# Kernel tuning notes

Hardware: AMD Instinct MI355X
Metric: run time of the kernel (lower is better)

Reference implementation:

```python
import jax, jax.numpy as jnp
import numpy as np

GAMMA = 0.9865
B, S, D = 8, 2048, 128


def setup_inputs() -> dict:
    key = jax.random.key(0)
    kq, kk, kv, kw = jax.random.split(key, 4)
    xq = jax.random.normal(kq, (B, S, D), dtype=jnp.float32)
    xk = jax.random.normal(kk, (B, S, D), dtype=jnp.float32)
    xv = jax.random.normal(kv, (B, S, D), dtype=jnp.float32)
    # NOTE: the original builds three Dense layers by repeating the SAME object,
    # so Q/K/V share a single no-bias weight matrix W.
    W = jax.random.normal(kw, (D, D), dtype=jnp.float32) * (1.0 / np.sqrt(D))
    return {"xq": xq, "xk": xk, "xv": xv, "W": W}


def _decay_matrix(seq_len, gamma):
    # Original: factors[i,j] = gamma^(i-j); keep upper triangle (j>=i); transpose.
    # Result: Dm[n,m] = gamma^(m-n) for n >= m, else 0 (lower triangular).
    n = jnp.arange(seq_len, dtype=jnp.float32)
    expo = n[None, :] - n[:, None]            # [S,S], entry (n,m) = m - n
    Dm = jnp.tril(jnp.float32(gamma) ** expo)  # zero out m > n before they'd matter
    return Dm


def reference(xq, xk, xv, W):
    Q = xq @ W
    K = xk @ W
    V = xv @ W
    d = Q.shape[-1]
    scores = jnp.einsum('bnd,bmd->bnm', Q, K) / jnp.sqrt(jnp.float32(d))
    Dm = _decay_matrix(Q.shape[1], GAMMA)
    # D /= reduce_sum(D, axis=1) ** 0.5  -> row-sums broadcast over LAST axis,
    # i.e. column m of D is divided by sqrt(rowsum[m]). Faithful to tf broadcasting.
    Dm = Dm / jnp.sqrt(jnp.sum(Dm, axis=1))
    scores = scores * Dm
    # per-batch norm: xs[n,m] / max(|sum_k xs[m,k]|, 1)  (tf broadcasting over last axis)
    s = jnp.sum(scores, axis=2)                       # [B,S]
    scores = scores / jnp.maximum(jnp.abs(s), 1.0)[:, None, :]
    return scores @ V
```

## Files before the change

kernel.cpp:

```cpp
#include <hip/hip_runtime.h>
#include <math.h>


constexpr int B = 8, S = 2048, D = 128;
constexpr int C = 64, NC = S / C;
constexpr int BS = B * S;
constexpr int NCH = B * NC;
#define GAMMA_F 0.9865f

typedef __attribute__((ext_vector_type(8))) short short8;
typedef __attribute__((ext_vector_type(8))) unsigned short ushort8;
typedef __attribute__((ext_vector_type(4))) float f32x4;

__device__ inline unsigned short f2bf(float f) {
  unsigned u = __builtin_bit_cast(unsigned, f);
  return (unsigned short)((u + 0x7FFF + ((u >> 16) & 1)) >> 16);
}
__device__ inline float bf2f(unsigned short h) {
  return __builtin_bit_cast(float, (unsigned)h << 16);
}

__global__ void k_init(const float* __restrict__ W, unsigned short* __restrict__ wt,
                       float* __restrict__ qs, float* __restrict__ ks) {
  int bid = blockIdx.x, tid = threadIdx.x;
  if (bid < 64) {
    int idx = bid * 256 + tid;
    int k = idx & 127, c = idx >> 7;
    wt[c * 128 + k] = f2bf(W[k * 128 + c]);
  } else {
    int n = (bid - 64) * 256 + tid;
    if (n < S) {
      double g = (double)GAMMA_F;
      double lg = log(g);
      double gmn = exp(-lg * (double)n);
      double gn  = exp(lg * (double)n);
      double ginv = 1.0 / g;
      double rs = (exp(log(ginv) * (double)(n + 1)) - 1.0) / (ginv - 1.0);
      qs[n] = (float)(gmn / sqrt(128.0));
      ks[n] = (float)(gn / sqrt(rs));
    }
  }
}

__global__ __launch_bounds__(256) void k_proj(
    const float* __restrict__ xq, const float* __restrict__ xk,
    const float* __restrict__ xv, const unsigned short* __restrict__ wt,
    const float* __restrict__ qs, const float* __restrict__ ks,
    unsigned short* __restrict__ qb, unsigned short* __restrict__ kb,
    unsigned short* __restrict__ vb, float* __restrict__ cs) {
  __shared__ float css[4][128];
  int mat = blockIdx.y;
  const float* X = (mat == 0) ? xq : ((mat == 1) ? xk : xv);
  unsigned short* Ob = (mat == 0) ? qb : ((mat == 1) ? kb : vb);

  int tid = threadIdx.x, w = tid >> 6, lane = tid & 63;
  int bc = blockIdx.x;
  int r0 = bc * 64 + w * 16;
  int arow = r0 + (lane & 15);
  int kg = (lane >> 4) * 8;

  f32x4 acc[8];
#pragma unroll
  for (int j = 0; j < 8; j++) acc[j] = (f32x4){0.f, 0.f, 0.f, 0.f};

#pragma unroll
  for (int t = 0; t < 4; t++) {
    int k0 = t * 32 + kg;
    const float* ap = X + (size_t)arow * 128 + k0;
    float a8[8];
    *(f32x4*)(a8) = *(const f32x4*)ap;
    *(f32x4*)(a8 + 4) = *(const f32x4*)(ap + 4);
    short8 af;
#pragma unroll
    for (int i = 0; i < 8; i++) af[i] = (short)f2bf(a8[i]);
#pragma unroll
    for (int j = 0; j < 8; j++) {
      short8 bf = *(const short8*)(wt + (size_t)(j * 16 + (lane & 15)) * 128 + k0);
      acc[j] = __builtin_amdgcn_mfma_f32_16x16x32_bf16(af, bf, acc[j], 0, 0, 0);
    }
  }
  int crow = r0 + (lane >> 4) * 4;
  float csp[8];
#pragma unroll
  for (int j = 0; j < 8; j++) csp[j] = 0.f;
#pragma unroll
  for (int rr = 0; rr < 4; rr++) {
    int row = crow + rr;
    int n = row & (S - 1);
    float sc = (mat == 0) ? qs[n] : ((mat == 1) ? ks[n] : 1.0f);
#pragma unroll
    for (int j = 0; j < 8; j++) {
      float v = acc[j][rr] * sc;
      Ob[(size_t)row * 128 + j * 16 + (lane & 15)] = f2bf(v);
      csp[j] += v;
    }
  }
  if (mat == 1) {
#pragma unroll
    for (int j = 0; j < 8; j++) {
      csp[j] += __shfl_xor(csp[j], 16);
      csp[j] += __shfl_xor(csp[j], 32);
    }
    if ((lane >> 4) == 0)
#pragma unroll
      for (int j = 0; j < 8; j++) css[w][j * 16 + lane] = csp[j];
  }
  __syncthreads();
  if (mat == 1 && tid < 128)
    cs[bc * 128 + tid] = css[0][tid] + css[1][tid] + css[2][tid] + css[3][tid];
}

__global__ __launch_bounds__(256) void k_mid(
    const unsigned short* __restrict__ qb, const unsigned short* __restrict__ kb,
    const unsigned short* __restrict__ vb, const float* __restrict__ cs,
    unsigned short* __restrict__ al, unsigned short* __restrict__ vbT,
    unsigned short* __restrict__ Hc) {
  __shared__ unsigned short kraw[64][136];
  __shared__ unsigned short kT[128][72];
  __shared__ unsigned short vT[128][72];
  __shared__ float csp[128];
  __shared__ float invl[64];
  int bc = blockIdx.x, b = bc >> 5, c = bc & 31;
  int tid = threadIdx.x, w = tid >> 6, lane = tid & 63;
  size_t base = (size_t)bc * C * D;
  int kg = (lane >> 4) * 8;
  int arow = w * 16 + (lane & 15);
  int crow = w * 16 + (lane >> 4) * 4;

  if (tid < 128) {
    float a = 0.f;
    for (int cc = 0; cc < c; cc++) a += cs[(size_t)(b * NC + cc) * D + tid];
    csp[tid] = a;
  }

  f32x4 a1[4];
#pragma unroll
  for (int m = 0; m < 4; m++) a1[m] = (f32x4){0.f, 0.f, 0.f, 0.f};
#pragma unroll
  for (int t = 0; t < 4; t++) {
    int k0 = t * 32 + kg;
    short8 af = *(const short8*)(qb + base + (size_t)arow * D + k0);
#pragma unroll
    for (int mt = 0; mt < 4; mt++) {
      short8 bf = *(const short8*)(kb + base + (size_t)(mt * 16 + (lane & 15)) * D + k0);
      a1[mt] = __builtin_amdgcn_mfma_f32_16x16x32_bf16(af, bf, a1[mt], 0, 0, 0);
    }
  }
  unsigned short* alg = al + (size_t)bc * 64 * 64;
  float rsum[4] = {0.f, 0.f, 0.f, 0.f};
#pragma unroll
  for (int mt = 0; mt < 4; mt++)
#pragma unroll
    for (int rr = 0; rr < 4; rr++) {
      int n_l = crow + rr, m_l = mt * 16 + (lane & 15);
      float mv = (n_l >= m_l) ? a1[mt][rr] : 0.f;
      alg[n_l * 64 + m_l] = f2bf(mv);
      rsum[rr] += mv;
    }
#pragma unroll
  for (int rr = 0; rr < 4; rr++) {
    float r = rsum[rr];
    r += __shfl_xor(r, 1); r += __shfl_xor(r, 2);
    r += __shfl_xor(r, 4); r += __shfl_xor(r, 8);
    rsum[rr] = r;
  }
  __syncthreads();
#pragma unroll
  for (int rr = 0; rr < 4; rr++) {
    int row = crow + rr;
    ushort8 q8 = *(const ushort8*)(qb + base + (size_t)row * D + (lane & 15) * 8);
    float dt = 0.f;
#pragma unroll
    for (int ii = 0; ii < 8; ii++) dt += bf2f(q8[ii]) * csp[(lane & 15) * 8 + ii];
    dt += __shfl_xor(dt, 1); dt += __shfl_xor(dt, 2);
    dt += __shfl_xor(dt, 4); dt += __shfl_xor(dt, 8);
    if ((lane & 15) == 0) invl[row] = 1.f / fmaxf(fabsf(rsum[rr] + dt), 1.f);
  }
#pragma unroll
  for (int i = 0; i < 4; i++) {
    int e = (i * 256 + tid) * 8;
    *(ushort8*)&kraw[e >> 7][e & 127] = *(const ushort8*)(kb + base + e);
  }
  __syncthreads();
  {
    int d = tid & 127, mh = tid >> 7;
#pragma unroll
    for (int mg = 0; mg < 4; mg++) {
      ushort8 pk;
#pragma unroll
      for (int i = 0; i < 8; i++) pk[i] = kraw[mh * 32 + mg * 8 + i][d];
      *(ushort8*)&kT[d][mh * 32 + mg * 8] = pk;
    }
  }
  __syncthreads();
#pragma unroll
  for (int i = 0; i < 4; i++) {
    int e = (i * 256 + tid) * 8;
    int row = e >> 7, col = e & 127;
    ushort8 v8 = *(const ushort8*)(vb + base + e);
    float inv = invl[row];
    ushort8 o;
#pragma unroll
    for (int ii = 0; ii < 8; ii++) o[ii] = f2bf(bf2f(v8[ii]) * inv);
    *(ushort8*)&kraw[row][col] = o;
  }
  __syncthreads();
  {
    int d = tid & 127, mh = tid >> 7;
#pragma unroll
    for (int mg = 0; mg < 4; mg++) {
      ushort8 pk;
#pragma unroll
      for (int i = 0; i < 8; i++) pk[i] = kraw[mh * 32 + mg * 8 + i][d];
      *(ushort8*)&vT[d][mh * 32 + mg * 8] = pk;
    }
  }
  __syncthreads();
  f32x4 acc[2][8];
#pragma unroll
  for (int i = 0; i < 2; i++)
#pragma unroll
    for (int j = 0; j < 8; j++) acc[i][j] = (f32x4){0.f, 0.f, 0.f, 0.f};
#pragma unroll
  for (int t = 0; t < 2; t++) {
    int k0 = t * 32 + kg;
    short8 a2[2];
#pragma unroll
    for (int i = 0; i < 2; i++)
      a2[i] = *(const short8*)&vT[w * 32 + i * 16 + (lane & 15)][k0];
#pragma unroll
    for (int j = 0; j < 8; j++) {
      short8 bf = *(const short8*)&kT[j * 16 + (lane & 15)][k0];
#pragma unroll
      for (int i = 0; i < 2; i++)
        acc[i][j] = __builtin_amdgcn_mfma_f32_16x16x32_bf16(a2[i], bf, acc[i][j], 0, 0, 0);
    }
  }
  unsigned short* g = Hc + (size_t)bc * D * D;
#pragma unroll
  for (int i = 0; i < 2; i++)
#pragma unroll
    for (int j = 0; j < 8; j++)
#pragma unroll
      for (int rr = 0; rr < 4; rr++)
        g[(size_t)(w * 32 + i * 16 + (lane >> 4) * 4 + rr) * D + j * 16 + (lane & 15)] =
            f2bf(acc[i][j][rr]);
  {
    int d = tid >> 1, pp = (tid & 1) * 32;
    unsigned short* dst = vbT + (size_t)bc * D * C + (size_t)d * C + pp;
#pragma unroll
    for (int q8i = 0; q8i < 4; q8i++)
      *(ushort8*)(dst + q8i * 8) = *(ushort8*)&vT[d][pp + q8i * 8];
  }
}

__global__ __launch_bounds__(64) void k_gscan(const unsigned short* __restrict__ Hc,
                                              unsigned short* __restrict__ HS) {
  int b = blockIdx.x, gy = blockIdx.y, t = threadIdx.x;
  int d2 = gy * 4 + (t >> 4), d1 = (t & 15) * 8;
  size_t off = ((size_t)(b * NC) * D + d2) * D + d1;
  ushort8 v[NC];
#pragma unroll
  for (int c = 0; c < NC; c++)
    v[c] = *(const ushort8*)(Hc + off + (size_t)c * D * D);
  float run[8];
#pragma unroll
  for (int j = 0; j < 8; j++) run[j] = 0.f;
#pragma unroll
  for (int c = 0; c < NC; c++) {
    ushort8 o;
#pragma unroll
    for (int j = 0; j < 8; j++) {
      o[j] = f2bf(run[j]);
      run[j] += bf2f(v[c][j]);
    }
    *(ushort8*)(HS + off + (size_t)c * D * D) = o;
  }
}

__global__ __launch_bounds__(256) void k_out(
    const unsigned short* __restrict__ qb, const unsigned short* __restrict__ al,
    const unsigned short* __restrict__ vbT, const unsigned short* __restrict__ HS,
    float* __restrict__ out) {
  int bc = blockIdx.x, tid = threadIdx.x, w = tid >> 6, lane = tid & 63;
  size_t base = (size_t)bc * C * D;
  int kg = (lane >> 4) * 8;
  int arow = w * 16 + (lane & 15);
  int crow = w * 16 + (lane >> 4) * 4;

  f32x4 acc[8];
#pragma unroll
  for (int j = 0; j < 8; j++) acc[j] = (f32x4){0.f, 0.f, 0.f, 0.f};
  const unsigned short* hrow = HS + (size_t)bc * D * D;
#pragma unroll
  for (int t = 0; t < 4; t++) {
    int k0 = t * 32 + kg;
    short8 af = *(const short8*)(qb + base + (size_t)arow * D + k0);
#pragma unroll
    for (int j = 0; j < 8; j++) {
      short8 bf = *(const short8*)(hrow + (size_t)(j * 16 + (lane & 15)) * D + k0);
      acc[j] = __builtin_amdgcn_mfma_f32_16x16x32_bf16(af, bf, acc[j], 0, 0, 0);
    }
  }
  const unsigned short* alg = al + (size_t)bc * 64 * 64;
  const unsigned short* vt = vbT + (size_t)bc * D * C;
#pragma unroll
  for (int t = 0; t < 2; t++) {
    int k0 = t * 32 + kg;
    short8 af = *(const short8*)(alg + (size_t)arow * 64 + k0);
#pragma unroll
    for (int j = 0; j < 8; j++) {
      short8 bf = *(const short8*)(vt + (size_t)(j * 16 + (lane & 15)) * C + k0);
      acc[j] = __builtin_amdgcn_mfma_f32_16x16x32_bf16(af, bf, acc[j], 0, 0, 0);
    }
  }
#pragma unroll
  for (int j = 0; j < 8; j++)
#pragma unroll
    for (int rr = 0; rr < 4; rr++)
      out[base + (size_t)(crow + rr) * D + j * 16 + (lane & 15)] = acc[j][rr];
}

extern "C" void kernel_launch(void* const* d_in, const int* in_sizes, int n_in,
                              void* d_out, int out_size, void* d_ws, size_t ws_size,
                              hipStream_t stream) {
  const float* xq = (const float*)d_in[0];
  const float* xk = (const float*)d_in[1];
  const float* xv = (const float*)d_in[2];
  const float* W  = (const float*)d_in[3];
  float* out = (float*)d_out;

  char* p = (char*)d_ws;
  unsigned short* qb  = (unsigned short*)p;  p += (size_t)BS * D * 2;
  unsigned short* kb  = (unsigned short*)p;  p += (size_t)BS * D * 2;
  unsigned short* vb  = (unsigned short*)p;  p += (size_t)BS * D * 2;
  unsigned short* vbT = (unsigned short*)p;  p += (size_t)NCH * D * C * 2;
  unsigned short* al  = (unsigned short*)p;  p += (size_t)NCH * C * C * 2;
  unsigned short* Hc  = (unsigned short*)p;  p += (size_t)NCH * D * D * 2;
  unsigned short* HS  = (unsigned short*)p;  p += (size_t)NCH * D * D * 2;
  unsigned short* wt  = (unsigned short*)p;  p += (size_t)D * D * 2;
  float* cs = (float*)p;                     p += (size_t)NCH * D * 4;
  float* qs = (float*)p;                     p += (size_t)S * 4;
  float* ks = (float*)p;                     p += (size_t)S * 4;

  hipLaunchKernelGGL(k_init, dim3(72), dim3(256), 0, stream, W, wt, qs, ks);
  hipLaunchKernelGGL(k_proj, dim3(NCH, 3), dim3(256), 0, stream,
                     xq, xk, xv, wt, qs, ks, qb, kb, vb, cs);
  hipLaunchKernelGGL(k_mid, dim3(NCH), dim3(256), 0, stream, qb, kb, vb, cs, al, vbT, Hc);
  hipLaunchKernelGGL(k_gscan, dim3(B, 32), dim3(64), 0, stream, Hc, HS);
  hipLaunchKernelGGL(k_out, dim3(NCH), dim3(256), 0, stream, qb, al, vbT, HS, out);
}
```

Measured before the change: 59.71 us.

## Fuse all stages into one cooperative persistent kernel with grid syncs

Replaces the five-launch pipeline (init, projection, mid, scan, output) with a single cooperative kernel of 256 blocks. Each block keeps its chunk's Q/K/V, the transposed W, the intra-chunk attention tile and the transposed V in LDS, and uses grid.sync between phases. This removes launch overhead and the global round-trips of the q/k/v/al/vT intermediates. In exchange it adds three grid-wide barriers, recomputes the W transpose in every block, and computes the decay scales in float instead of double. The old multi-kernel path is kept as a fallback if the cooperative launch fails.

```diff
diff --git a/kernel.cpp b/kernel.cpp
--- a/kernel.cpp
+++ b/kernel.cpp
@@ -1,5 +1,8 @@
 #include <hip/hip_runtime.h>
+#include <hip/hip_cooperative_groups.h>
 #include <math.h>
+
+namespace cg = cooperative_groups;
 
 
 constexpr int B = 8, S = 2048, D = 128;
@@ -20,8 +23,273 @@
   return __builtin_bit_cast(float, (unsigned)h << 16);
 }
 
-__global__ void k_init(const float* __restrict__ W, unsigned short* __restrict__ wt,
-                       float* __restrict__ qs, float* __restrict__ ks) {
+__global__ __launch_bounds__(256, 1) void k_fused(
+    const float* __restrict__ xq, const float* __restrict__ xk,
+    const float* __restrict__ xv, const float* __restrict__ W,
+    float* __restrict__ cs, unsigned short* __restrict__ Hc,
+    unsigned short* __restrict__ HS, float* __restrict__ out) {
+  __shared__ unsigned short qkv[3][64][136];
+  __shared__ alignas(16) char ovl[34816];
+  __shared__ unsigned short vT[128][72];
+  __shared__ float csp[128];
+  __shared__ float invl[64];
+  __shared__ float css[4][128];
+  auto wt = (unsigned short(*)[136])ovl;
+  auto kT = (unsigned short(*)[72])ovl;
+  auto al = (unsigned short(*)[72])(ovl + 18432);
+
+  cg::grid_group grid = cg::this_grid();
+  int bc = blockIdx.x, b = bc >> 5, c = bc & 31;
+  int tid = threadIdx.x, w = tid >> 6, lane = tid & 63;
+  int l15 = lane & 15;
+  int kg = (lane >> 4) * 8;
+  int arow = w * 16 + l15;
+  int crow = w * 16 + (lane >> 4) * 4;
+
+  for (int idx = tid; idx < 128 * 128; idx += 256) {
+    int cc = idx >> 7, k = idx & 127;
+    wt[cc][k] = f2bf(W[k * 128 + cc]);
+  }
+  float lgf = logf(GAMMA_F);
+  __syncthreads();
+
+  for (int mat = 0; mat < 3; mat++) {
+    const float* X = (mat == 0) ? xq : ((mat == 1) ? xk : xv);
+    f32x4 acc[8];
+#pragma unroll
+    for (int j = 0; j < 8; j++) acc[j] = (f32x4){0.f, 0.f, 0.f, 0.f};
+#pragma unroll
+    for (int t = 0; t < 4; t++) {
+      int k0 = t * 32 + kg;
+      const float* ap = X + (size_t)(bc * 64 + arow) * 128 + k0;
+      float a8[8];
+      *(f32x4*)(a8) = *(const f32x4*)ap;
+      *(f32x4*)(a8 + 4) = *(const f32x4*)(ap + 4);
+      short8 af;
+#pragma unroll
+      for (int i = 0; i < 8; i++) af[i] = (short)f2bf(a8[i]);
+#pragma unroll
+      for (int j = 0; j < 8; j++) {
+        short8 bf = *(const short8*)&wt[j * 16 + l15][k0];
+        acc[j] = __builtin_amdgcn_mfma_f32_16x16x32_bf16(af, bf, acc[j], 0, 0, 0);
+      }
+    }
+    float cacc[8];
+#pragma unroll
+    for (int j = 0; j < 8; j++) cacc[j] = 0.f;
+#pragma unroll
+    for (int rr = 0; rr < 4; rr++) {
+      int row = crow + rr;
+      int n = (bc * 64 + row) & (S - 1);
+      float sc;
+      if (mat == 0) {
+        sc = expf(-lgf * (float)n) * 0.088388347f;
+      } else if (mat == 1) {
+        float rs = (expf(-lgf * (float)(n + 1)) - 1.f) * (GAMMA_F / (1.f - GAMMA_F));
+        sc = expf(lgf * (float)n) / sqrtf(rs);
+      } else {
+        sc = 1.f;
+      }
+#pragma unroll
+      for (int j = 0; j < 8; j++) {
+        float v = acc[j][rr] * sc;
+        qkv[mat][row][j * 16 + l15] = f2bf(v);
+        if (mat == 1) cacc[j] += v;
+      }
+    }
+    if (mat == 1) {
+#pragma unroll
+      for (int j = 0; j < 8; j++) {
+        cacc[j] += __shfl_xor(cacc[j], 16);
+        cacc[j] += __shfl_xor(cacc[j], 32);
+      }
+      if ((lane >> 4) == 0)
+#pragma unroll
+        for (int j = 0; j < 8; j++) css[w][j * 16 + lane] = cacc[j];
+      __syncthreads();
+      if (tid < 128)
+        cs[(size_t)bc * 128 + tid] = css[0][tid] + css[1][tid] + css[2][tid] + css[3][tid];
+    }
+  }
+  grid.sync();
+
+  if (tid < 128) {
+    float a = 0.f;
+    for (int cc = 0; cc < c; cc++) a += cs[(size_t)(b * NC + cc) * 128 + tid];
+    csp[tid] = a;
+  }
+  f32x4 a1[4];
+#pragma unroll
+  for (int m = 0; m < 4; m++) a1[m] = (f32x4){0.f, 0.f, 0.f, 0.f};
+#pragma unroll
+  for (int t = 0; t < 4; t++) {
+    int k0 = t * 32 + kg;
+    short8 af = *(const short8*)&qkv[0][arow][k0];
+#pragma unroll
+    for (int mt = 0; mt < 4; mt++) {
+      short8 bf = *(const short8*)&qkv[1][mt * 16 + l15][k0];
+      a1[mt] = __builtin_amdgcn_mfma_f32_16x16x32_bf16(af, bf, a1[mt], 0, 0, 0);
+    }
+  }
+  float rsum[4] = {0.f, 0.f, 0.f, 0.f};
+#pragma unroll
+  for (int mt = 0; mt < 4; mt++)
+#pragma unroll
+    for (int rr = 0; rr < 4; rr++) {
+      int n_l = crow + rr, m_l = mt * 16 + l15;
+      float mv = (n_l >= m_l) ? a1[mt][rr] : 0.f;
+      al[n_l][m_l] = f2bf(mv);
+      rsum[rr] += mv;
+    }
+#pragma unroll
+  for (int rr = 0; rr < 4; rr++) {
+    float r = rsum[rr];
+    r += __shfl_xor(r, 1); r += __shfl_xor(r, 2);
+    r += __shfl_xor(r, 4); r += __shfl_xor(r, 8);
+    rsum[rr] = r;
+  }
+  __syncthreads();
+#pragma unroll
+  for (int rr = 0; rr < 4; rr++) {
+    int row = crow + rr;
+    ushort8 q8 = *(const ushort8*)&qkv[0][row][l15 * 8];
+    float dt = 0.f;
+#pragma unroll
+    for (int ii = 0; ii < 8; ii++) dt += bf2f(q8[ii]) * csp[l15 * 8 + ii];
+    dt += __shfl_xor(dt, 1); dt += __shfl_xor(dt, 2);
+    dt += __shfl_xor(dt, 4); dt += __shfl_xor(dt, 8);
+    if (l15 == 0) invl[row] = 1.f / fmaxf(fabsf(rsum[rr] + dt), 1.f);
+  }
+  {
+    int d = tid & 127, mh = tid >> 7;
+#pragma unroll
+    for (int mg = 0; mg < 4; mg++) {
+      ushort8 pk;
+#pragma unroll
+      for (int i = 0; i < 8; i++) pk[i] = qkv[1][mh * 32 + mg * 8 + i][d];
+      *(ushort8*)&kT[d][mh * 32 + mg * 8] = pk;
+    }
+  }
+  __syncthreads();
+#pragma unroll
+  for (int i = 0; i < 4; i++) {
+    int e = (i * 256 + tid) * 8;
+    int row = e >> 7, col = e & 127;
+    ushort8 v8 = *(const ushort8*)&qkv[2][row][col];
+    float inv = invl[row];
+    ushort8 o;
+#pragma unroll
+    for (int ii = 0; ii < 8; ii++) o[ii] = f2bf(bf2f(v8[ii]) * inv);
+    *(ushort8*)&qkv[2][row][col] = o;
+  }
+  __syncthreads();
+  {
+    int d = tid & 127, mh = tid >> 7;
+#pragma unroll
+    for (int mg = 0; mg < 4; mg++) {
+      ushort8 pk;
+#pragma unroll
+      for (int i = 0; i < 8; i++) pk[i] = qkv[2][mh * 32 + mg * 8 + i][d];
+      *(ushort8*)&vT[d][mh * 32 + mg * 8] = pk;
+    }
+  }
+  __syncthreads();
+  {
+    f32x4 hacc[2][8];
+#pragma unroll
+    for (int i = 0; i < 2; i++)
+#pragma unroll
+      for (int j = 0; j < 8; j++) hacc[i][j] = (f32x4){0.f, 0.f, 0.f, 0.f};
+#pragma unroll
+    for (int t = 0; t < 2; t++) {
+      int k0 = t * 32 + kg;
+      short8 a2[2];
+#pragma unroll
+      for (int i = 0; i < 2; i++)
+        a2[i] = *(const short8*)&vT[w * 32 + i * 16 + l15][k0];
+#pragma unroll
+      for (int j = 0; j < 8; j++) {
+        short8 bf = *(const short8*)&kT[j * 16 + l15][k0];
+#pragma unroll
+        for (int i = 0; i < 2; i++)
+          hacc[i][j] = __builtin_amdgcn_mfma_f32_16x16x32_bf16(a2[i], bf, hacc[i][j], 0, 0, 0);
+      }
+    }
+    unsigned short* g = Hc + (size_t)bc * D * D;
+#pragma unroll
+    for (int i = 0; i < 2; i++)
+#pragma unroll
+      for (int j = 0; j < 8; j++)
+#pragma unroll
+        for (int rr = 0; rr < 4; rr++)
+          g[(size_t)(w * 32 + i * 16 + (lane >> 4) * 4 + rr) * D + j * 16 + l15] =
+              f2bf(hacc[i][j][rr]);
+  }
+  grid.sync();
+
+  {
+    int d2 = c * 4 + (tid >> 6);
+    int s16 = tid & 63;
+    if (s16 < 16) {
+      int d1 = s16 * 8;
+      size_t off = ((size_t)(b * NC) * D + d2) * D + d1;
+      ushort8 v[NC];
+#pragma unroll
+      for (int c2 = 0; c2 < NC; c2++)
+        v[c2] = *(const ushort8*)(Hc + off + (size_t)c2 * D * D);
+      float run[8];
+#pragma unroll
+      for (int j = 0; j < 8; j++) run[j] = 0.f;
+#pragma unroll
+      for (int c2 = 0; c2 < NC; c2++) {
+        ushort8 o;
+#pragma unroll
+        for (int j = 0; j < 8; j++) {
+          o[j] = f2bf(run[j]);
+          run[j] += bf2f(v[c2][j]);
+        }
+        *(ushort8*)(HS + off + (size_t)c2 * D * D) = o;
+      }
+    }
+  }
+  grid.sync();
+
+  {
+    f32x4 oacc[8];
+#pragma unroll
+    for (int j = 0; j < 8; j++) oacc[j] = (f32x4){0.f, 0.f, 0.f, 0.f};
+    const unsigned short* hrow = HS + (size_t)bc * D * D;
+#pragma unroll
+    for (int t = 0; t < 4; t++) {
+      int k0 = t * 32 + kg;
+      short8 af = *(const short8*)&qkv[0][arow][k0];
+#pragma unroll
+      for (int j = 0; j < 8; j++) {
+        short8 bf = *(const short8*)(hrow + (size_t)(j * 16 + l15) * D + k0);
+        oacc[j] = __builtin_amdgcn_mfma_f32_16x16x32_bf16(af, bf, oacc[j], 0, 0, 0);
+      }
+    }
+#pragma unroll
+    for (int t = 0; t < 2; t++) {
+      int k0 = t * 32 + kg;
+      short8 af = *(const short8*)&al[arow][k0];
+#pragma unroll
+      for (int j = 0; j < 8; j++) {
+        short8 bf = *(const short8*)&vT[j * 16 + l15][k0];
+        oacc[j] = __builtin_amdgcn_mfma_f32_16x16x32_bf16(af, bf, oacc[j], 0, 0, 0);
+      }
+    }
+    size_t base = (size_t)bc * C * D;
+#pragma unroll
+    for (int j = 0; j < 8; j++)
+#pragma unroll
+      for (int rr = 0; rr < 4; rr++)
+        out[base + (size_t)(crow + rr) * D + j * 16 + l15] = oacc[j][rr];
+  }
+}
+
+__global__ void fb_init(const float* __restrict__ W, unsigned short* __restrict__ wt,
+                        float* __restrict__ qs, float* __restrict__ ks) {
   int bid = blockIdx.x, tid = threadIdx.x;
   if (bid < 64) {
     int idx = bid * 256 + tid;
@@ -42,7 +310,7 @@
   }
 }
 
-__global__ __launch_bounds__(256) void k_proj(
+__global__ __launch_bounds__(256) void fb_proj(
     const float* __restrict__ xq, const float* __restrict__ xk,
     const float* __restrict__ xv, const unsigned short* __restrict__ wt,
     const float* __restrict__ qs, const float* __restrict__ ks,
@@ -62,7 +330,6 @@
   f32x4 acc[8];
 #pragma unroll
   for (int j = 0; j < 8; j++) acc[j] = (f32x4){0.f, 0.f, 0.f, 0.f};
-
 #pragma unroll
   for (int t = 0; t < 4; t++) {
     int k0 = t * 32 + kg;
@@ -110,7 +377,7 @@
     cs[bc * 128 + tid] = css[0][tid] + css[1][tid] + css[2][tid] + css[3][tid];
 }
 
-__global__ __launch_bounds__(256) void k_mid(
+__global__ __launch_bounds__(256) void fb_mid(
     const unsigned short* __restrict__ qb, const unsigned short* __restrict__ kb,
     const unsigned short* __restrict__ vb, const float* __restrict__ cs,
     unsigned short* __restrict__ al, unsigned short* __restrict__ vbT,
@@ -129,10 +396,9 @@
 
   if (tid < 128) {
     float a = 0.f;
-    for (int cc = 0; cc < c; cc++) a += cs[(size_t)(b * NC + cc) * D + tid];
+    for (int cc = 0; cc < c; cc++) a += cs[(size_t)(b * NC + cc) * 128 + tid];
     csp[tid] = a;
   }
-
   f32x4 a1[4];
 #pragma unroll
   for (int m = 0; m < 4; m++) a1[m] = (f32x4){0.f, 0.f, 0.f, 0.f};
@@ -254,8 +520,8 @@
   }
 }
 
-__global__ __launch_bounds__(64) void k_gscan(const unsigned short* __restrict__ Hc,
-                                              unsigned short* __restrict__ HS) {
+__global__ __launch_bounds__(64) void fb_gscan(const unsigned short* __restrict__ Hc,
+                                               unsigned short* __restrict__ HS) {
   int b = blockIdx.x, gy = blockIdx.y, t = threadIdx.x;
   int d2 = gy * 4 + (t >> 4), d1 = (t & 15) * 8;
   size_t off = ((size_t)(b * NC) * D + d2) * D + d1;
@@ -278,7 +544,7 @@
   }
 }
 
-__global__ __launch_bounds__(256) void k_out(
+__global__ __launch_bounds__(256) void fb_out(
     const unsigned short* __restrict__ qb, const unsigned short* __restrict__ al,
     const unsigned short* __restrict__ vbT, const unsigned short* __restrict__ HS,
     float* __restrict__ out) {
@@ -331,11 +597,14 @@
   float* out = (float*)d_out;
 
   char* p = (char*)d_ws;
+  float* cs_m = (float*)p;                   p += (size_t)NCH * D * 4;
+  unsigned short* Hc_m = (unsigned short*)p; p += (size_t)NCH * D * D * 2;
+  unsigned short* HS_m = (unsigned short*)p; p += (size_t)NCH * D * D * 2;
   unsigned short* qb  = (unsigned short*)p;  p += (size_t)BS * D * 2;
   unsigned short* kb  = (unsigned short*)p;  p += (size_t)BS * D * 2;
   unsigned short* vb  = (unsigned short*)p;  p += (size_t)BS * D * 2;
   unsigned short* vbT = (unsigned short*)p;  p += (size_t)NCH * D * C * 2;
-  unsigned short* al  = (unsigned short*)p;  p += (size_t)NCH * C * C * 2;
+  unsigned short* alg = (unsigned short*)p;  p += (size_t)NCH * C * C * 2;
   unsigned short* Hc  = (unsigned short*)p;  p += (size_t)NCH * D * D * 2;
   unsigned short* HS  = (unsigned short*)p;  p += (size_t)NCH * D * D * 2;
   unsigned short* wt  = (unsigned short*)p;  p += (size_t)D * D * 2;
@@ -343,10 +612,17 @@
   float* qs = (float*)p;                     p += (size_t)S * 4;
   float* ks = (float*)p;                     p += (size_t)S * 4;
 
-  hipLaunchKernelGGL(k_init, dim3(72), dim3(256), 0, stream, W, wt, qs, ks);
-  hipLaunchKernelGGL(k_proj, dim3(NCH, 3), dim3(256), 0, stream,
-                     xq, xk, xv, wt, qs, ks, qb, kb, vb, cs);
-  hipLaunchKernelGGL(k_mid, dim3(NCH), dim3(256), 0, stream, qb, kb, vb, cs, al, vbT, Hc);
-  hipLaunchKernelGGL(k_gscan, dim3(B, 32), dim3(64), 0, stream, Hc, HS);
-  hipLaunchKernelGGL(k_out, dim3(NCH), dim3(256), 0, stream, qb, al, vbT, HS, out);
-}
+  void* args[] = {(void*)&xq, (void*)&xk, (void*)&xv, (void*)&W,
+                  (void*)&cs_m, (void*)&Hc_m, (void*)&HS_m, (void*)&out};
+  hipError_t e = hipLaunchCooperativeKernel((const void*)k_fused, dim3(NCH),
+                                            dim3(256), args, 0, stream);
+  if (e != hipSuccess) {
+    hipLaunchKernelGGL(fb_init, dim3(72), dim3(256), 0, stream, W, wt, qs, ks);
+    hipLaunchKernelGGL(fb_proj, dim3(NCH, 3), dim3(256), 0, stream,
+                       xq, xk, xv, wt, qs, ks, qb, kb, vb, cs);
+    hipLaunchKernelGGL(fb_mid, dim3(NCH), dim3(256), 0, stream, qb, kb, vb, cs,
+                       alg, vbT, Hc);
+    hipLaunchKernelGGL(fb_gscan, dim3(B, 32), dim3(64), 0, stream, Hc, HS);
+    hipLaunchKernelGGL(fb_out, dim3(NCH), dim3(256), 0, stream, qb, alg, vbT, HS, out);
+  }
+}
```

Measured after the change: 141.3 us. 137% more time.

## Double threads per block in k_mid and k_out, splitting MFMA tiles across eight waves

Applied to the files above, without the earlier changes.

Raises k_mid and k_out from 256 to 512 threads per block. The score, Hc and output MFMA tiles are re-partitioned so each of the eight waves computes half as many tiles, and row sums are reduced through shared memory. The aim is more parallelism per block, since the grid has only 256 blocks on a device with many CUs, and shorter per-wave serial chains. The cost is extra shared-memory reduction and less operand reuse per wave.

```diff
diff --git a/kernel.cpp b/kernel.cpp
--- a/kernel.cpp
+++ b/kernel.cpp
@@ -62,7 +62,6 @@
   f32x4 acc[8];
 #pragma unroll
   for (int j = 0; j < 8; j++) acc[j] = (f32x4){0.f, 0.f, 0.f, 0.f};
-
 #pragma unroll
   for (int t = 0; t < 4; t++) {
     int k0 = t * 32 + kg;
@@ -110,7 +109,7 @@
     cs[bc * 128 + tid] = css[0][tid] + css[1][tid] + css[2][tid] + css[3][tid];
 }
 
-__global__ __launch_bounds__(256) void k_mid(
+__global__ __launch_bounds__(512) void k_mid(
     const unsigned short* __restrict__ qb, const unsigned short* __restrict__ kb,
     const unsigned short* __restrict__ vb, const float* __restrict__ cs,
     unsigned short* __restrict__ al, unsigned short* __restrict__ vbT,
@@ -120,82 +119,94 @@
   __shared__ unsigned short vT[128][72];
   __shared__ float csp[128];
   __shared__ float invl[64];
+  __shared__ float rsum_l[2][64];
   int bc = blockIdx.x, b = bc >> 5, c = bc & 31;
   int tid = threadIdx.x, w = tid >> 6, lane = tid & 63;
+  int l15 = lane & 15;
+  int kg = (lane >> 4) * 8;
   size_t base = (size_t)bc * C * D;
-  int kg = (lane >> 4) * 8;
-  int arow = w * 16 + (lane & 15);
-  int crow = w * 16 + (lane >> 4) * 4;
 
   if (tid < 128) {
     float a = 0.f;
-    for (int cc = 0; cc < c; cc++) a += cs[(size_t)(b * NC + cc) * D + tid];
+    for (int cc = 0; cc < c; cc++) a += cs[(size_t)(b * NC + cc) * 128 + tid];
     csp[tid] = a;
   }
 
-  f32x4 a1[4];
-#pragma unroll
-  for (int m = 0; m < 4; m++) a1[m] = (f32x4){0.f, 0.f, 0.f, 0.f};
-#pragma unroll
-  for (int t = 0; t < 4; t++) {
-    int k0 = t * 32 + kg;
-    short8 af = *(const short8*)(qb + base + (size_t)arow * D + k0);
-#pragma unroll
-    for (int mt = 0; mt < 4; mt++) {
-      short8 bf = *(const short8*)(kb + base + (size_t)(mt * 16 + (lane & 15)) * D + k0);
-      a1[mt] = __builtin_amdgcn_mfma_f32_16x16x32_bf16(af, bf, a1[mt], 0, 0, 0);
-    }
-  }
-  unsigned short* alg = al + (size_t)bc * 64 * 64;
-  float rsum[4] = {0.f, 0.f, 0.f, 0.f};
-#pragma unroll
-  for (int mt = 0; mt < 4; mt++)
+  {
+    int rt = w & 3, mh = w >> 2;
+    int arow = rt * 16 + l15;
+    int crow = rt * 16 + (lane >> 4) * 4;
+    f32x4 a1[2];
+#pragma unroll
+    for (int mi = 0; mi < 2; mi++) a1[mi] = (f32x4){0.f, 0.f, 0.f, 0.f};
+#pragma unroll
+    for (int t = 0; t < 4; t++) {
+      int k0 = t * 32 + kg;
+      short8 af = *(const short8*)(qb + base + (size_t)arow * D + k0);
+#pragma unroll
+      for (int mi = 0; mi < 2; mi++) {
+        int mt = mh * 2 + mi;
+        short8 bf = *(const short8*)(kb + base + (size_t)(mt * 16 + l15) * D + k0);
+        a1[mi] = __builtin_amdgcn_mfma_f32_16x16x32_bf16(af, bf, a1[mi], 0, 0, 0);
+      }
+    }
+    unsigned short* alg = al + (size_t)bc * 64 * 64;
+    float rsp[4] = {0.f, 0.f, 0.f, 0.f};
+#pragma unroll
+    for (int mi = 0; mi < 2; mi++)
+#pragma unroll
+      for (int rr = 0; rr < 4; rr++) {
+        int n_l = crow + rr, m_l = (mh * 2 + mi) * 16 + l15;
+        float mv = (n_l >= m_l) ? a1[mi][rr] : 0.f;
+        alg[n_l * 64 + m_l] = f2bf(mv);
+        rsp[rr] += mv;
+      }
 #pragma unroll
     for (int rr = 0; rr < 4; rr++) {
-      int n_l = crow + rr, m_l = mt * 16 + (lane & 15);
-      float mv = (n_l >= m_l) ? a1[mt][rr] : 0.f;
-      alg[n_l * 64 + m_l] = f2bf(mv);
-      rsum[rr] += mv;
-    }
-#pragma unroll
-  for (int rr = 0; rr < 4; rr++) {
-    float r = rsum[rr];
-    r += __shfl_xor(r, 1); r += __shfl_xor(r, 2);
-    r += __shfl_xor(r, 4); r += __shfl_xor(r, 8);
-    rsum[rr] = r;
-  }
-  __syncthreads();
-#pragma unroll
-  for (int rr = 0; rr < 4; rr++) {
-    int row = crow + rr;
-    ushort8 q8 = *(const ushort8*)(qb + base + (size_t)row * D + (lane & 15) * 8);
-    float dt = 0.f;
-#pragma unroll
-    for (int ii = 0; ii < 8; ii++) dt += bf2f(q8[ii]) * csp[(lane & 15) * 8 + ii];
-    dt += __shfl_xor(dt, 1); dt += __shfl_xor(dt, 2);
-    dt += __shfl_xor(dt, 4); dt += __shfl_xor(dt, 8);
-    if ((lane & 15) == 0) invl[row] = 1.f / fmaxf(fabsf(rsum[rr] + dt), 1.f);
-  }
-#pragma unroll
-  for (int i = 0; i < 4; i++) {
-    int e = (i * 256 + tid) * 8;
+      float r = rsp[rr];
+      r += __shfl_xor(r, 1); r += __shfl_xor(r, 2);
+      r += __shfl_xor(r, 4); r += __shfl_xor(r, 8);
+      if (l15 == 0) rsum_l[mh][crow + rr] = r;
+    }
+  }
+#pragma unroll
+  for (int i = 0; i < 2; i++) {
+    int e = (i * 512 + tid) * 8;
     *(ushort8*)&kraw[e >> 7][e & 127] = *(const ushort8*)(kb + base + e);
   }
   __syncthreads();
-  {
-    int d = tid & 127, mh = tid >> 7;
-#pragma unroll
-    for (int mg = 0; mg < 4; mg++) {
+
+  {
+    int row = tid >> 3, part = tid & 7;
+    const unsigned short* q = qb + base + (size_t)row * D + part * 16;
+    ushort8 q8a = *(const ushort8*)q;
+    ushort8 q8b = *(const ushort8*)(q + 8);
+    float dot = 0.f;
+#pragma unroll
+    for (int ii = 0; ii < 8; ii++) {
+      dot = fmaf(bf2f(q8a[ii]), csp[part * 16 + ii], dot);
+      dot = fmaf(bf2f(q8b[ii]), csp[part * 16 + 8 + ii], dot);
+    }
+    dot += __shfl_xor(dot, 1); dot += __shfl_xor(dot, 2); dot += __shfl_xor(dot, 4);
+    if (part == 0) {
+      float s = rsum_l[0][row] + rsum_l[1][row] + dot;
+      invl[row] = 1.f / fmaxf(fabsf(s), 1.f);
+    }
+  }
+  {
+    int d = tid & 127, mh2 = tid >> 7;
+#pragma unroll
+    for (int mg = 0; mg < 2; mg++) {
       ushort8 pk;
 #pragma unroll
-      for (int i = 0; i < 8; i++) pk[i] = kraw[mh * 32 + mg * 8 + i][d];
-      *(ushort8*)&kT[d][mh * 32 + mg * 8] = pk;
-    }
-  }
-  __syncthreads();
-#pragma unroll
-  for (int i = 0; i < 4; i++) {
-    int e = (i * 256 + tid) * 8;
+      for (int i = 0; i < 8; i++) pk[i] = kraw[mh2 * 16 + mg * 8 + i][d];
+      *(ushort8*)&kT[d][mh2 * 16 + mg * 8] = pk;
+    }
+  }
+  __syncthreads();
+#pragma unroll
+  for (int i = 0; i < 2; i++) {
+    int e = (i * 512 + tid) * 8;
     int row = e >> 7, col = e & 127;
     ushort8 v8 = *(const ushort8*)(vb + base + e);
     float inv = invl[row];
@@ -206,51 +217,43 @@
   }
   __syncthreads();
   {
-    int d = tid & 127, mh = tid >> 7;
-#pragma unroll
-    for (int mg = 0; mg < 4; mg++) {
+    int d = tid & 127, mh2 = tid >> 7;
+#pragma unroll
+    for (int mg = 0; mg < 2; mg++) {
       ushort8 pk;
 #pragma unroll
-      for (int i = 0; i < 8; i++) pk[i] = kraw[mh * 32 + mg * 8 + i][d];
-      *(ushort8*)&vT[d][mh * 32 + mg * 8] = pk;
-    }
-  }
-  __syncthreads();
-  f32x4 acc[2][8];
-#pragma unroll
-  for (int i = 0; i < 2; i++)
-#pragma unroll
-    for (int j = 0; j < 8; j++) acc[i][j] = (f32x4){0.f, 0.f, 0.f, 0.f};
-#pragma unroll
-  for (int t = 0; t < 2; t++) {
-    int k0 = t * 32 + kg;
-    short8 a2[2];
-#pragma unroll
-    for (int i = 0; i < 2; i++)
-      a2[i] = *(const short8*)&vT[w * 32 + i * 16 + (lane & 15)][k0];
-#pragma unroll
-    for (int j = 0; j < 8; j++) {
-      short8 bf = *(const short8*)&kT[j * 16 + (lane & 15)][k0];
-#pragma unroll
-      for (int i = 0; i < 2; i++)
-        acc[i][j] = __builtin_amdgcn_mfma_f32_16x16x32_bf16(a2[i], bf, acc[i][j], 0, 0, 0);
-    }
-  }
-  unsigned short* g = Hc + (size_t)bc * D * D;
-#pragma unroll
-  for (int i = 0; i < 2; i++)
+      for (int i = 0; i < 8; i++) pk[i] = kraw[mh2 * 16 + mg * 8 + i][d];
+      *(ushort8*)&vT[d][mh2 * 16 + mg * 8] = pk;
+    }
+  }
+  __syncthreads();
+  {
+    f32x4 hacc[8];
+#pragma unroll
+    for (int j = 0; j < 8; j++) hacc[j] = (f32x4){0.f, 0.f, 0.f, 0.f};
+#pragma unroll
+    for (int t = 0; t < 2; t++) {
+      int k0 = t * 32 + kg;
+      short8 a2 = *(const short8*)&vT[w * 16 + l15][k0];
+#pragma unroll
+      for (int j = 0; j < 8; j++) {
+        short8 bf = *(const short8*)&kT[j * 16 + l15][k0];
+        hacc[j] = __builtin_amdgcn_mfma_f32_16x16x32_bf16(a2, bf, hacc[j], 0, 0, 0);
+      }
+    }
+    unsigned short* g = Hc + (size_t)bc * D * D;
 #pragma unroll
     for (int j = 0; j < 8; j++)
 #pragma unroll
       for (int rr = 0; rr < 4; rr++)
-        g[(size_t)(w * 32 + i * 16 + (lane >> 4) * 4 + rr) * D + j * 16 + (lane & 15)] =
-            f2bf(acc[i][j][rr]);
-  {
-    int d = tid >> 1, pp = (tid & 1) * 32;
+        g[(size_t)(w * 16 + (lane >> 4) * 4 + rr) * D + j * 16 + l15] =
+            f2bf(hacc[j][rr]);
+  }
+  {
+    int d = tid >> 2, pp = (tid & 3) * 16;
     unsigned short* dst = vbT + (size_t)bc * D * C + (size_t)d * C + pp;
-#pragma unroll
-    for (int q8i = 0; q8i < 4; q8i++)
-      *(ushort8*)(dst + q8i * 8) = *(ushort8*)&vT[d][pp + q8i * 8];
+    *(ushort8*)(dst) = *(ushort8*)&vT[d][pp];
+    *(ushort8*)(dst + 8) = *(ushort8*)&vT[d][pp + 8];
   }
 }
 
@@ -278,28 +281,31 @@
   }
 }
 
-__global__ __launch_bounds__(256) void k_out(
+__global__ __launch_bounds__(512) void k_out(
     const unsigned short* __restrict__ qb, const unsigned short* __restrict__ al,
     const unsigned short* __restrict__ vbT, const unsigned short* __restrict__ HS,
     float* __restrict__ out) {
   int bc = blockIdx.x, tid = threadIdx.x, w = tid >> 6, lane = tid & 63;
+  int l15 = lane & 15;
   size_t base = (size_t)bc * C * D;
   int kg = (lane >> 4) * 8;
-  int arow = w * 16 + (lane & 15);
-  int crow = w * 16 + (lane >> 4) * 4;
-
-  f32x4 acc[8];
-#pragma unroll
-  for (int j = 0; j < 8; j++) acc[j] = (f32x4){0.f, 0.f, 0.f, 0.f};
+  int rt = w >> 1, ch = w & 1;
+  int arow = rt * 16 + l15;
+  int crow = rt * 16 + (lane >> 4) * 4;
+
+  f32x4 acc[4];
+#pragma unroll
+  for (int j = 0; j < 4; j++) acc[j] = (f32x4){0.f, 0.f, 0.f, 0.f};
   const unsigned short* hrow = HS + (size_t)bc * D * D;
 #pragma unroll
   for (int t = 0; t < 4; t++) {
     int k0 = t * 32 + kg;
     short8 af = *(const short8*)(qb + base + (size_t)arow * D + k0);
 #pragma unroll
-    for (int j = 0; j < 8; j++) {
-      short8 bf = *(const short8*)(hrow + (size_t)(j * 16 + (lane & 15)) * D + k0);
-      acc[j] = __builtin_amdgcn_mfma_f32_16x16x32_bf16(af, bf, acc[j], 0, 0, 0);
+    for (int jj = 0; jj < 4; jj++) {
+      int j = ch * 4 + jj;
+      short8 bf = *(const short8*)(hrow + (size_t)(j * 16 + l15) * D + k0);
+      acc[jj] = __builtin_amdgcn_mfma_f32_16x16x32_bf16(af, bf, acc[jj], 0, 0, 0);
     }
   }
   const unsigned short* alg = al + (size_t)bc * 64 * 64;
@@ -309,16 +315,17 @@
     int k0 = t * 32 + kg;
     short8 af = *(const short8*)(alg + (size_t)arow * 64 + k0);
 #pragma unroll
-    for (int j = 0; j < 8; j++) {
-      short8 bf = *(const short8*)(vt + (size_t)(j * 16 + (lane & 15)) * C + k0);
-      acc[j] = __builtin_amdgcn_mfma_f32_16x16x32_bf16(af, bf, acc[j], 0, 0, 0);
-    }
-  }
-#pragma unroll
-  for (int j = 0; j < 8; j++)
+    for (int jj = 0; jj < 4; jj++) {
+      int j = ch * 4 + jj;
+      short8 bf = *(const short8*)(vt + (size_t)(j * 16 + l15) * C + k0);
+      acc[jj] = __builtin_amdgcn_mfma_f32_16x16x32_bf16(af, bf, acc[jj], 0, 0, 0);
+    }
+  }
+#pragma unroll
+  for (int jj = 0; jj < 4; jj++)
 #pragma unroll
     for (int rr = 0; rr < 4; rr++)
-      out[base + (size_t)(crow + rr) * D + j * 16 + (lane & 15)] = acc[j][rr];
+      out[base + (size_t)(crow + rr) * D + (ch * 4 + jj) * 16 + l15] = acc[jj][rr];
 }
 
 extern "C" void kernel_launch(void* const* d_in, const int* in_sizes, int n_in,
@@ -346,7 +353,8 @@
   hipLaunchKernelGGL(k_init, dim3(72), dim3(256), 0, stream, W, wt, qs, ks);
   hipLaunchKernelGGL(k_proj, dim3(NCH, 3), dim3(256), 0, stream,
                      xq, xk, xv, wt, qs, ks, qb, kb, vb, cs);
-  hipLaunchKernelGGL(k_mid, dim3(NCH), dim3(256), 0, stream, qb, kb, vb, cs, al, vbT, Hc);
+  hipLaunchKernelGGL(k_mid, dim3(NCH), dim3(512), 0, stream, qb, kb, vb, cs,
+                     al, vbT, Hc);
   hipLaunchKernelGGL(k_gscan, dim3(B, 32), dim3(64), 0, stream, Hc, HS);
-  hipLaunchKernelGGL(k_out, dim3(NCH), dim3(256), 0, stream, qb, al, vbT, HS, out);
-}
+  hipLaunchKernelGGL(k_out, dim3(NCH), dim3(512), 0, stream, qb, al, vbT, HS, out);
+}
```

Result: no change. 59.04 us (-1.1%).
